# Kernel tuning notes

Measured on AMD Instinct MI355X. Metric: run time of the kernel, lower is better.

Reference implementation:

```python
import jax, jax.numpy as jnp
import numpy as np

N_NODES = 50000
N_EDGES = 800000
IN_FEAT = 1000
HID = 128
HEADS = 2
NEG_SLOPE = 0.2  # PyG GATConv default
EPS = 1e-16      # PyG softmax denom eps


def setup_inputs() -> dict:
    key = jax.random.key(0)
    ks = jax.random.split(key, 12)
    x = jax.random.normal(ks[0], (N_NODES, IN_FEAT), dtype=jnp.float32)
    edge_index = jax.random.randint(ks[1], (2, N_EDGES), 0, N_NODES, dtype=jnp.int64)
    readout_idx = jax.random.randint(ks[2], (1024,), 0, N_NODES, dtype=jnp.int64)
    s = 0.05
    return {
        "x": x,
        "edge_index": edge_index,
        "readout_idx": readout_idx,
        "W1": jax.random.normal(ks[3], (IN_FEAT, HEADS * HID), dtype=jnp.float32) * s,
        "att_src1": jax.random.normal(ks[4], (HEADS, HID), dtype=jnp.float32) * s,
        "att_dst1": jax.random.normal(ks[5], (HEADS, HID), dtype=jnp.float32) * s,
        "b1": jax.random.normal(ks[6], (HEADS * HID,), dtype=jnp.float32) * s,
        "W2": jax.random.normal(ks[7], (HEADS * HID, 1), dtype=jnp.float32) * s,
        "att_src2": jax.random.normal(ks[8], (1, 1), dtype=jnp.float32) * s,
        "att_dst2": jax.random.normal(ks[9], (1, 1), dtype=jnp.float32) * s,
        "b2": jax.random.normal(ks[10], (1,), dtype=jnp.float32) * s,
    }


def gat_conv(x, edge_index, W, att_src, att_dst, bias, heads, out_dim, concat):
    """PyG GATConv with add_self_loops=False. x: [N, F_in]."""
    n = x.shape[0]
    src, dst = edge_index[0], edge_index[1]
    h = (x @ W).reshape(n, heads, out_dim)            # [N, H, D]
    a_src = jnp.einsum("nhd,hd->nh", h, att_src)      # [N, H]
    a_dst = jnp.einsum("nhd,hd->nh", h, att_dst)
    e = jax.nn.leaky_relu(a_src[src] + a_dst[dst], NEG_SLOPE)  # [E, H]
    # softmax over incoming edges of each destination node
    e_max = jax.ops.segment_max(e, dst, num_segments=n)
    e_exp = jnp.exp(e - e_max[dst])
    denom = jax.ops.segment_sum(e_exp, dst, num_segments=n)
    alpha = e_exp / (denom[dst] + EPS)                # [E, H]
    msg = h[src] * alpha[:, :, None]                  # [E, H, D]
    out = jax.ops.segment_sum(msg, dst, num_segments=n)  # [N, H, D]
    out = out.reshape(n, heads * out_dim) if concat else out.mean(axis=1)
    return out + bias


def reference(x, edge_index, readout_idx, W1, att_src1, att_dst1, b1,
              W2, att_src2, att_dst2, b2):
    # dropout is identity in eval mode
    h = gat_conv(x, edge_index, W1, att_src1, att_dst1, b1, HEADS, HID, True)
    h = jax.nn.relu(h)
    out = gat_conv(h, edge_index, W2, att_src2, att_dst2, b2, 1, 1, False)  # [N, 1]
    return out[readout_idx]  # [1024, 1]
```

## Files before the change

kernel.cpp:

```cpp
#include <hip/hip_runtime.h>
#include <hip/hip_bf16.h>
#include <math.h>

#define N_NODES 50000
#define N_EDGES 800000
#define IN_FEAT 1000
#define HID 128
#define HEADS 2
#define FOUT 256
#define NEG_SLOPE 0.2f
#define EPS 1e-16f

#define KPAD 1024
#define GEMM_NWG 782

typedef __bf16 bf16x8 __attribute__((ext_vector_type(8)));
typedef float f32x4 __attribute__((ext_vector_type(4)));

__device__ __forceinline__ float lrelu(float v) { return v > 0.f ? v : NEG_SLOPE * v; }

__device__ __forceinline__ ushort bf16rn(float v) {
  union { float f; unsigned u; } a; a.f = v;
  unsigned r = a.u + 0x7FFFu + ((a.u >> 16) & 1u);
  return (ushort)(r >> 16);
}

__device__ __forceinline__ void gload_lds16(const void* g, void* l) {
  __builtin_amdgcn_global_load_lds((const __attribute__((address_space(1))) void*)g,
                                   (__attribute__((address_space(3))) void*)l, 16, 0, 0);
}

__global__ void hist_kernel(const int* __restrict__ dst, int* __restrict__ counts) {
  int e = blockIdx.x * blockDim.x + threadIdx.x;
  if (e < N_EDGES) atomicAdd(&counts[dst[e]], 1);
}

__global__ __launch_bounds__(1024) void scan1_kernel(const int* __restrict__ counts,
                                                     int* __restrict__ iscan,
                                                     int* __restrict__ bsum) {
  __shared__ int buf[1024];
  const int t = threadIdx.x;
  const int i = blockIdx.x * 1024 + t;
  int v = (i < N_NODES) ? counts[i] : 0;
  buf[t] = v;
  __syncthreads();
#pragma unroll
  for (int off = 1; off < 1024; off <<= 1) {
    int x = (t >= off) ? buf[t - off] : 0;
    __syncthreads();
    buf[t] += x;
    __syncthreads();
  }
  if (i < N_NODES) iscan[i] = buf[t];
  if (t == 1023) bsum[blockIdx.x] = buf[1023];
}

__global__ __launch_bounds__(64) void scan2_kernel(const int* __restrict__ bsum,
                                                   int* __restrict__ boff,
                                                   int* __restrict__ row_start, int nblk) {
  const int t = threadIdx.x;
  int v = (t < nblk) ? bsum[t] : 0;
  int s = v;
#pragma unroll
  for (int off = 1; off < 64; off <<= 1) {
    int y = __shfl_up(s, off, 64);
    if (t >= off) s += y;
  }
  if (t < nblk) boff[t] = s - v;
  if (t == nblk - 1) row_start[N_NODES] = s;
}

__global__ void scan3_kernel(const int* __restrict__ iscan, const int* __restrict__ counts,
                             const int* __restrict__ boff, int* __restrict__ row_start,
                             int* __restrict__ cursor) {
  int i = blockIdx.x * blockDim.x + threadIdx.x;
  if (i < N_NODES) {
    int rs = boff[i >> 10] + iscan[i] - counts[i];
    row_start[i] = rs;
    cursor[i] = rs;
  }
}

__global__ void scatter_kernel(const int* __restrict__ src, const int* __restrict__ dst,
                               int* __restrict__ cursor, int* __restrict__ csr_src) {
  int e = blockIdx.x * blockDim.x + threadIdx.x;
  if (e < N_EDGES) {
    int pos = atomicAdd(&cursor[dst[e]], 1);
    csr_src[pos] = src[e];
  }
}

__global__ __launch_bounds__(256) void cvtB1_kernel(const float* __restrict__ B,
                                                    ushort* __restrict__ Bt) {
  int i = blockIdx.x * 256 + threadIdx.x;
  int nn = i >> 8;
  int k4 = (i & 255) << 2;
  ushort4 h;
#pragma unroll
  for (int j = 0; j < 4; ++j) {
    int k = k4 + j;
    float v = (k < IN_FEAT) ? B[(size_t)k * FOUT + nn] : 0.f;
    ((ushort*)&h)[j] = bf16rn(v);
  }
  *(ushort4*)(Bt + (size_t)nn * KPAD + k4) = h;
}

__global__ __launch_bounds__(256, 2) void gemm_fused2_kernel(
    const float* __restrict__ X, const ushort* __restrict__ Bt,
    float* __restrict__ C) {
  __shared__ ushort lB[2][128 * 64];

  const int orig = blockIdx.x;
  const int q = GEMM_NWG >> 3, r = GEMM_NWG & 7;
  const int xcd = orig & 7, idx = orig >> 3;
  const int lin = (xcd < r) ? xcd * (q + 1) + idx : r * (q + 1) + (xcd - r) * q + idx;
  const int brow = (lin >> 1) * 128;
  const int bcol = (lin & 1) * 128;

  const int t = threadIdx.x;
  const int lane = t & 63, wid = t >> 6;
  const int fr = lane & 15, g = lane >> 4;
  const int wrow = wid * 32;

  float4 areg[2][2][2];

  auto loadA = [&](int ks) {
#pragma unroll
    for (int m = 0; m < 2; ++m)
#pragma unroll
      for (int h = 0; h < 2; ++h) {
        const int row = brow + wrow + m * 16 + fr;
        const int k = ks * 64 + h * 32 + g * 8;
        if (row < N_NODES && k < IN_FEAT) {
          const float* p = X + (size_t)row * IN_FEAT + k;
          areg[m][h][0] = *(const float4*)p;
          areg[m][h][1] = *(const float4*)(p + 4);
        } else {
          areg[m][h][0] = make_float4(0.f, 0.f, 0.f, 0.f);
          areg[m][h][1] = make_float4(0.f, 0.f, 0.f, 0.f);
        }
      }
  };

  auto stageB = [&](int ks, int buf) {
    const int k0b = ks * 128;
#pragma unroll
    for (int i = 0; i < 4; ++i) {
      int u = i * 256 + t;
      int row = u >> 3;
      int inner = (u & 7) * 16;
      int soff = inner ^ ((row & 7) << 4);
      size_t boff = (size_t)(bcol + row) * (KPAD * 2) + k0b + soff;
      gload_lds16((const char*)Bt + boff, (char*)&lB[buf][0] + u * 16);
    }
  };

  f32x4 acc[2][8];
  const f32x4 z4 = {0.f, 0.f, 0.f, 0.f};
#pragma unroll
  for (int m = 0; m < 2; ++m)
#pragma unroll
    for (int n = 0; n < 8; ++n) acc[m][n] = z4;

  stageB(0, 0);
  loadA(0);
  const int NK = KPAD / 64;
  for (int ks = 0; ks < NK; ++ks) {
    bf16x8 ah[2][2], al[2][2];
#pragma unroll
    for (int m = 0; m < 2; ++m)
#pragma unroll
      for (int h = 0; h < 2; ++h) {
        const float* vv = (const float*)&areg[m][h][0];
        bf16x8 hv, lv;
#pragma unroll
        for (int j = 0; j < 8; ++j) {
          float v = vv[j];
          unsigned u = __float_as_uint(v);
          ((ushort*)&hv)[j] = (ushort)(u >> 16);
          float hf = __uint_as_float(u & 0xFFFF0000u);
          float d = v - hf;
          ((ushort*)&lv)[j] = (ushort)(__float_as_uint(d) >> 16);
        }
        ah[m][h] = hv;
        al[m][h] = lv;
      }
    if (ks + 1 < NK) {
      loadA(ks + 1);
      asm volatile("s_waitcnt vmcnt(8)" ::: "memory");
    } else {
      asm volatile("s_waitcnt vmcnt(0)" ::: "memory");
    }
    __builtin_amdgcn_sched_barrier(0);
    __builtin_amdgcn_s_barrier();
    __builtin_amdgcn_sched_barrier(0);
    if (ks + 1 < NK) stageB(ks + 1, (ks + 1) & 1);
    const int buf = ks & 1;
#pragma unroll
    for (int h = 0; h < 2; ++h) {
      bf16x8 bfrag[8];
#pragma unroll
      for (int n = 0; n < 8; ++n) {
        int row = n * 16 + fr;
        int off = row * 128 + ((h * 64 + g * 16) ^ ((row & 7) << 4));
        bfrag[n] = *(const bf16x8*)((const char*)&lB[buf][0] + off);
      }
#pragma unroll
      for (int m = 0; m < 2; ++m)
#pragma unroll
        for (int n = 0; n < 8; ++n) {
          acc[m][n] = __builtin_amdgcn_mfma_f32_16x16x32_bf16(ah[m][h], bfrag[n], acc[m][n], 0, 0, 0);
          acc[m][n] = __builtin_amdgcn_mfma_f32_16x16x32_bf16(al[m][h], bfrag[n], acc[m][n], 0, 0, 0);
        }
    }
  }

#pragma unroll
  for (int m = 0; m < 2; ++m) {
    int rowbase = brow + wrow + m * 16 + g * 4;
#pragma unroll
    for (int n = 0; n < 8; ++n) {
      int col = bcol + n * 16 + fr;
#pragma unroll
      for (int rr = 0; rr < 4; ++rr) {
        int row = rowbase + rr;
        if (row < N_NODES) C[(size_t)row * FOUT + col] = acc[m][n][rr];
      }
    }
  }
}

__global__ __launch_bounds__(64) void att1_kernel(const float* __restrict__ h1,
                                                  const float* __restrict__ as,
                                                  const float* __restrict__ ad,
                                                  float* __restrict__ asrc,
                                                  float* __restrict__ adst) {
  const int n = blockIdx.x;
  const int lane = threadIdx.x;
  const float* hr = h1 + (size_t)n * FOUT;
  float4 hv = *(const float4*)(hr + 4 * lane);
  float4 sv = *(const float4*)(as + 4 * lane);
  float4 dv = *(const float4*)(ad + 4 * lane);
  float ps = hv.x * sv.x + hv.y * sv.y + hv.z * sv.z + hv.w * sv.w;
  float pd = hv.x * dv.x + hv.y * dv.y + hv.z * dv.z + hv.w * dv.w;
#pragma unroll
  for (int off = 16; off > 0; off >>= 1) {
    ps += __shfl_xor(ps, off, 64);
    pd += __shfl_xor(pd, off, 64);
  }
  if ((lane & 31) == 0) {
    int hh = lane >> 5;
    asrc[2 * n + hh] = ps;
    adst[2 * n + hh] = pd;
  }
}

__global__ __launch_bounds__(64) void agg1_kernel(
    const float* __restrict__ h1, const float* __restrict__ asrc,
    const float* __restrict__ adst, const int* __restrict__ row_start,
    const int* __restrict__ csr_src, const float* __restrict__ b1,
    const float* __restrict__ W2, float* __restrict__ z) {
  const int n = blockIdx.x;
  const int lane = threadIdx.x;
  const bool head0 = lane < 32;
  const float ad0 = adst[2 * n], ad1 = adst[2 * n + 1];
  const int jb = row_start[n], je = row_start[n + 1];
  float ax = 0.f, ay = 0.f, az = 0.f, aw = 0.f;
  float m0 = -INFINITY, m1 = -INFINITY, s0 = 0.f, s1 = 0.f;

  for (int base = jb; base < je; base += 64) {
    int cnt = je - base;
    if (cnt > 64) cnt = 64;
    const bool act = lane < cnt;
    const int sr = csr_src[base + (act ? lane : 0)];
    float e0 = -INFINITY, e1 = -INFINITY;
    if (act) {
      const float2 av = *(const float2*)(asrc + 2 * sr);
      e0 = lrelu(av.x + ad0);
      e1 = lrelu(av.y + ad1);
    }
    float c0 = e0, c1 = e1;
#pragma unroll
    for (int off = 32; off > 0; off >>= 1) {
      c0 = fmaxf(c0, __shfl_xor(c0, off, 64));
      c1 = fmaxf(c1, __shfl_xor(c1, off, 64));
    }
    const float m0n = fmaxf(m0, c0), m1n = fmaxf(m1, c1);
    const float f0 = __expf(m0 - m0n), f1 = __expf(m1 - m1n);
    const float p0 = act ? __expf(e0 - m0n) : 0.f;
    const float p1 = act ? __expf(e1 - m1n) : 0.f;
    float t0 = p0, t1 = p1;
#pragma unroll
    for (int off = 32; off > 0; off >>= 1) {
      t0 += __shfl_xor(t0, off, 64);
      t1 += __shfl_xor(t1, off, 64);
    }
    s0 = s0 * f0 + t0;
    s1 = s1 * f1 + t1;
    m0 = m0n;
    m1 = m1n;
    const float f = head0 ? f0 : f1;
    ax *= f; ay *= f; az *= f; aw *= f;
    for (int j = 0; j < cnt; ++j) {
      const int srj = __shfl(sr, j, 64);
      const float pj0 = __shfl(p0, j, 64);
      const float pj1 = __shfl(p1, j, 64);
      const float pj = head0 ? pj0 : pj1;
      float4 hv = *(const float4*)(h1 + (size_t)srj * FOUT + 4 * lane);
      ax = fmaf(pj, hv.x, ax);
      ay = fmaf(pj, hv.y, ay);
      az = fmaf(pj, hv.z, az);
      aw = fmaf(pj, hv.w, aw);
    }
  }
  const float inv = head0 ? 1.f / (s0 + EPS) : 1.f / (s1 + EPS);
  float4 bv = *(const float4*)(b1 + 4 * lane);
  float4 wv = *(const float4*)(W2 + 4 * lane);
  float r0 = fmaxf(fmaf(ax, inv, bv.x), 0.f);
  float r1 = fmaxf(fmaf(ay, inv, bv.y), 0.f);
  float r2 = fmaxf(fmaf(az, inv, bv.z), 0.f);
  float r3 = fmaxf(fmaf(aw, inv, bv.w), 0.f);
  float part = r0 * wv.x + r1 * wv.y + r2 * wv.z + r3 * wv.w;
#pragma unroll
  for (int off = 32; off > 0; off >>= 1) part += __shfl_xor(part, off, 64);
  if (lane == 0) z[n] = part;
}

__global__ __launch_bounds__(64) void agg2_kernel(
    const float* __restrict__ z, const int* __restrict__ row_start,
    const int* __restrict__ csr_src, const float* __restrict__ as2p,
    const float* __restrict__ ad2p, const float* __restrict__ b2p,
    float* __restrict__ out2) {
  const int n = blockIdx.x;
  const int lane = threadIdx.x;
  const float as2 = as2p[0], ad2 = ad2p[0], b2 = b2p[0];
  const float adz = z[n] * ad2;
  const int jb = row_start[n], je = row_start[n + 1];
  float m = -INFINITY, s = 0.f, num = 0.f;
  for (int base = jb; base < je; base += 64) {
    int cnt = je - base;
    if (cnt > 64) cnt = 64;
    const bool act = lane < cnt;
    const int sr = csr_src[base + (act ? lane : 0)];
    const float zs = act ? z[sr] : 0.f;
    const float e = act ? lrelu(zs * as2 + adz) : -INFINITY;
    float c = e;
#pragma unroll
    for (int off = 32; off > 0; off >>= 1) c = fmaxf(c, __shfl_xor(c, off, 64));
    const float mn = fmaxf(m, c);
    const float f = __expf(m - mn);
    const float p = act ? __expf(e - mn) : 0.f;
    float tp = p, tz = p * zs;
#pragma unroll
    for (int off = 32; off > 0; off >>= 1) {
      tp += __shfl_xor(tp, off, 64);
      tz += __shfl_xor(tz, off, 64);
    }
    s = s * f + tp;
    num = num * f + tz;
    m = mn;
  }
  if (lane == 0) out2[n] = num / (s + EPS) + b2;
}

__global__ void readout_kernel(const float* __restrict__ out2, const int* __restrict__ ridx,
                               float* __restrict__ out, int n) {
  int i = blockIdx.x * blockDim.x + threadIdx.x;
  if (i < n) out[i] = out2[ridx[i]];
}

extern "C" void kernel_launch(void* const* d_in, const int* in_sizes, int n_in,
                              void* d_out, int out_size, void* d_ws, size_t ws_size,
                              hipStream_t stream) {
  const float* x   = (const float*)d_in[0];
  const int* ei    = (const int*)d_in[1];
  const int* ridx  = (const int*)d_in[2];
  const float* W1  = (const float*)d_in[3];
  const float* as1 = (const float*)d_in[4];
  const float* ad1 = (const float*)d_in[5];
  const float* b1  = (const float*)d_in[6];
  const float* W2  = (const float*)d_in[7];
  const float* as2 = (const float*)d_in[8];
  const float* ad2 = (const float*)d_in[9];
  const float* b2  = (const float*)d_in[10];
  float* out = (float*)d_out;

  char* ws = (char*)d_ws;
  size_t off = 0;
  auto alloc = [&](size_t bytes) -> void* {
    void* p = ws + off;
    off += (bytes + 255) & ~(size_t)255;
    return p;
  };
  float* h1   = (float*)alloc((size_t)N_NODES * FOUT * 4);
  float* asrc = (float*)alloc((size_t)N_NODES * 2 * 4);
  float* adst = (float*)alloc((size_t)N_NODES * 2 * 4);
  float* z    = (float*)alloc((size_t)N_NODES * 4);
  float* out2 = (float*)alloc((size_t)N_NODES * 4);
  int* counts = (int*)alloc((size_t)N_NODES * 4);
  int* rowst  = (int*)alloc((size_t)(N_NODES + 1) * 4);
  int* cursor = (int*)alloc((size_t)N_NODES * 4);
  int* csr    = (int*)alloc((size_t)N_EDGES * 4);
  int* iscan  = (int*)alloc((size_t)N_NODES * 4);
  int* bsum   = (int*)alloc(64 * 4);
  int* boff   = (int*)alloc(64 * 4);
  ushort* Bt  = (ushort*)alloc((size_t)FOUT * KPAD * 2);

  const int* src = ei;
  const int* dst = ei + N_EDGES;
  const int nblk = (N_NODES + 1023) / 1024;

  hipMemsetAsync(counts, 0, (size_t)N_NODES * 4, stream);
  hist_kernel<<<(N_EDGES + 255) / 256, 256, 0, stream>>>(dst, counts);
  scan1_kernel<<<nblk, 1024, 0, stream>>>(counts, iscan, bsum);
  scan2_kernel<<<1, 64, 0, stream>>>(bsum, boff, rowst, nblk);
  scan3_kernel<<<(N_NODES + 255) / 256, 256, 0, stream>>>(iscan, counts, boff, rowst, cursor);
  scatter_kernel<<<(N_EDGES + 255) / 256, 256, 0, stream>>>(src, dst, cursor, csr);

  cvtB1_kernel<<<256, 256, 0, stream>>>(W1, Bt);
  gemm_fused2_kernel<<<GEMM_NWG, 256, 0, stream>>>(x, Bt, h1);

  att1_kernel<<<N_NODES, 64, 0, stream>>>(h1, as1, ad1, asrc, adst);
  agg1_kernel<<<N_NODES, 64, 0, stream>>>(h1, asrc, adst, rowst, csr, b1, W2, z);
  agg2_kernel<<<N_NODES, 64, 0, stream>>>(z, rowst, csr, as2, ad2, b2, out2);
  readout_kernel<<<4, 256, 0, stream>>>(out2, ridx, out, out_size);
}
```

Baseline: 579.8 us.

## Fuse attention logits into LDS-free GEMM with full-width row tiles

The GEMM drops LDS staging of the bf16 weight tile. Each wave now loads its B fragments straight from global memory with register double-buffering, and the A tile is double-buffered across k steps. Each 512-thread block covers a 128-row by 256-column tile, so every X row is read once instead of twice, which halves the grid. The per-node attention dot products are computed from the accumulators in the epilogue with lane shuffles, so the separate att1 kernel and its re-read of h1 go away. The cost is that B is fetched redundantly from global/L2 by every wave, and the larger block with more live registers may lower occupancy.

```diff
diff --git a/kernel.cpp b/kernel.cpp
--- a/kernel.cpp
+++ b/kernel.cpp
@@ -12,7 +12,7 @@
 #define EPS 1e-16f
 
 #define KPAD 1024
-#define GEMM_NWG 782
+#define GEMM_NWG 391
 
 typedef __bf16 bf16x8 __attribute__((ext_vector_type(8)));
 typedef float f32x4 __attribute__((ext_vector_type(4)));
@@ -23,11 +23,6 @@
   union { float f; unsigned u; } a; a.f = v;
   unsigned r = a.u + 0x7FFFu + ((a.u >> 16) & 1u);
   return (ushort)(r >> 16);
-}
-
-__device__ __forceinline__ void gload_lds16(const void* g, void* l) {
-  __builtin_amdgcn_global_load_lds((const __attribute__((address_space(1))) void*)g,
-                                   (__attribute__((address_space(3))) void*)l, 16, 0, 0);
 }
 
 __global__ void hist_kernel(const int* __restrict__ dst, int* __restrict__ counts) {
@@ -105,56 +100,26 @@
   *(ushort4*)(Bt + (size_t)nn * KPAD + k4) = h;
 }
 
-__global__ __launch_bounds__(256, 2) void gemm_fused2_kernel(
+__global__ __launch_bounds__(512, 2) void gemm_nolds_kernel(
     const float* __restrict__ X, const ushort* __restrict__ Bt,
-    float* __restrict__ C) {
-  __shared__ ushort lB[2][128 * 64];
-
+    const float* __restrict__ as1, const float* __restrict__ ad1,
+    float* __restrict__ C, float* __restrict__ asrc, float* __restrict__ adst) {
+  const int q = GEMM_NWG >> 3, r = GEMM_NWG & 7;
   const int orig = blockIdx.x;
-  const int q = GEMM_NWG >> 3, r = GEMM_NWG & 7;
   const int xcd = orig & 7, idx = orig >> 3;
   const int lin = (xcd < r) ? xcd * (q + 1) + idx : r * (q + 1) + (xcd - r) * q + idx;
-  const int brow = (lin >> 1) * 128;
-  const int bcol = (lin & 1) * 128;
-
-  const int t = threadIdx.x;
-  const int lane = t & 63, wid = t >> 6;
+  const int brow = lin * 128;
+
+  const int t = threadIdx.x, lane = t & 63, wid = t >> 6;
+  const int wc = wid & 1;
+  const int wrow = (wid >> 1) * 32;
   const int fr = lane & 15, g = lane >> 4;
-  const int wrow = wid * 32;
-
-  float4 areg[2][2][2];
-
-  auto loadA = [&](int ks) {
-#pragma unroll
-    for (int m = 0; m < 2; ++m)
-#pragma unroll
-      for (int h = 0; h < 2; ++h) {
-        const int row = brow + wrow + m * 16 + fr;
-        const int k = ks * 64 + h * 32 + g * 8;
-        if (row < N_NODES && k < IN_FEAT) {
-          const float* p = X + (size_t)row * IN_FEAT + k;
-          areg[m][h][0] = *(const float4*)p;
-          areg[m][h][1] = *(const float4*)(p + 4);
-        } else {
-          areg[m][h][0] = make_float4(0.f, 0.f, 0.f, 0.f);
-          areg[m][h][1] = make_float4(0.f, 0.f, 0.f, 0.f);
-        }
-      }
-  };
-
-  auto stageB = [&](int ks, int buf) {
-    const int k0b = ks * 128;
-#pragma unroll
-    for (int i = 0; i < 4; ++i) {
-      int u = i * 256 + t;
-      int row = u >> 3;
-      int inner = (u & 7) * 16;
-      int soff = inner ^ ((row & 7) << 4);
-      size_t boff = (size_t)(bcol + row) * (KPAD * 2) + k0b + soff;
-      gload_lds16((const char*)Bt + boff, (char*)&lB[buf][0] + u * 16);
-    }
-  };
-
+  const int row0 = brow + wrow + fr;
+  const int NK = KPAD / 64;
+
+  float4 aA[2][2][2], aB[2][2][2];
+  bf16x8 bfA[8], bfB[8];
+  bf16x8 ah[2][2], al[2][2];
   f32x4 acc[2][8];
   const f32x4 z4 = {0.f, 0.f, 0.f, 0.f};
 #pragma unroll
@@ -162,16 +127,38 @@
 #pragma unroll
     for (int n = 0; n < 8; ++n) acc[m][n] = z4;
 
-  stageB(0, 0);
-  loadA(0);
-  const int NK = KPAD / 64;
-  for (int ks = 0; ks < NK; ++ks) {
-    bf16x8 ah[2][2], al[2][2];
+  auto loadA = [&](int ks, float4 (&d)[2][2][2]) {
+#pragma unroll
+    for (int m = 0; m < 2; ++m) {
+      int rr = row0 + m * 16;
+      int rc = rr < N_NODES ? rr : N_NODES - 1;
+      const float* base = X + (size_t)rc * IN_FEAT;
+#pragma unroll
+      for (int h = 0; h < 2; ++h) {
+        int k = ks * 64 + h * 32 + g * 8;
+        if (k < IN_FEAT) {
+          d[m][h][0] = *(const float4*)(base + k);
+          d[m][h][1] = *(const float4*)(base + k + 4);
+        } else {
+          d[m][h][0] = make_float4(0.f, 0.f, 0.f, 0.f);
+          d[m][h][1] = make_float4(0.f, 0.f, 0.f, 0.f);
+        }
+      }
+    }
+  };
+  auto loadB = [&](int ks, int h, bf16x8 (&bf)[8]) {
+#pragma unroll
+    for (int n = 0; n < 8; ++n) {
+      const ushort* p = Bt + (size_t)(wc * 128 + n * 16 + fr) * KPAD + ks * 64 + h * 32 + g * 8;
+      bf[n] = *(const bf16x8*)p;
+    }
+  };
+  auto cvt = [&](const float4 (&s)[2][2][2]) {
 #pragma unroll
     for (int m = 0; m < 2; ++m)
 #pragma unroll
       for (int h = 0; h < 2; ++h) {
-        const float* vv = (const float*)&areg[m][h][0];
+        const float* vv = (const float*)&s[m][h][0];
         bf16x8 hv, lv;
 #pragma unroll
         for (int j = 0; j < 8; ++j) {
@@ -179,79 +166,77 @@
           unsigned u = __float_as_uint(v);
           ((ushort*)&hv)[j] = (ushort)(u >> 16);
           float hf = __uint_as_float(u & 0xFFFF0000u);
-          float d = v - hf;
-          ((ushort*)&lv)[j] = (ushort)(__float_as_uint(d) >> 16);
+          ((ushort*)&lv)[j] = (ushort)(__float_as_uint(v - hf) >> 16);
         }
         ah[m][h] = hv;
         al[m][h] = lv;
       }
-    if (ks + 1 < NK) {
-      loadA(ks + 1);
-      asm volatile("s_waitcnt vmcnt(8)" ::: "memory");
-    } else {
-      asm volatile("s_waitcnt vmcnt(0)" ::: "memory");
-    }
-    __builtin_amdgcn_sched_barrier(0);
-    __builtin_amdgcn_s_barrier();
-    __builtin_amdgcn_sched_barrier(0);
-    if (ks + 1 < NK) stageB(ks + 1, (ks + 1) & 1);
-    const int buf = ks & 1;
-#pragma unroll
-    for (int h = 0; h < 2; ++h) {
-      bf16x8 bfrag[8];
+  };
+  auto mmac = [&](int h, bf16x8 (&bf)[8]) {
+#pragma unroll
+    for (int m = 0; m < 2; ++m)
 #pragma unroll
       for (int n = 0; n < 8; ++n) {
-        int row = n * 16 + fr;
-        int off = row * 128 + ((h * 64 + g * 16) ^ ((row & 7) << 4));
-        bfrag[n] = *(const bf16x8*)((const char*)&lB[buf][0] + off);
-      }
-#pragma unroll
-      for (int m = 0; m < 2; ++m)
-#pragma unroll
-        for (int n = 0; n < 8; ++n) {
-          acc[m][n] = __builtin_amdgcn_mfma_f32_16x16x32_bf16(ah[m][h], bfrag[n], acc[m][n], 0, 0, 0);
-          acc[m][n] = __builtin_amdgcn_mfma_f32_16x16x32_bf16(al[m][h], bfrag[n], acc[m][n], 0, 0, 0);
-        }
-    }
-  }
+        acc[m][n] = __builtin_amdgcn_mfma_f32_16x16x32_bf16(ah[m][h], bf[n], acc[m][n], 0, 0, 0);
+        acc[m][n] = __builtin_amdgcn_mfma_f32_16x16x32_bf16(al[m][h], bf[n], acc[m][n], 0, 0, 0);
+      }
+  };
+  auto step = [&](float4 (&cur)[2][2][2], float4 (&nxt)[2][2][2], int ks) {
+    cvt(cur);
+    if (ks + 1 < NK) loadA(ks + 1, nxt);
+    loadB(ks, 1, bfB);
+    mmac(0, bfA);
+    if (ks + 1 < NK) loadB(ks + 1, 0, bfA);
+    mmac(1, bfB);
+  };
+
+  loadA(0, aA);
+  loadB(0, 0, bfA);
+  for (int k2 = 0; k2 < NK; k2 += 2) {
+    step(aA, aB, k2);
+    step(aB, aA, k2 + 1);
+  }
+
+  float ws8[8], wd8[8];
+#pragma unroll
+  for (int n = 0; n < 8; ++n) {
+    ws8[n] = as1[wc * 128 + n * 16 + fr];
+    wd8[n] = ad1[wc * 128 + n * 16 + fr];
+  }
+#pragma unroll
+  for (int m = 0; m < 2; ++m)
+#pragma unroll
+    for (int rr = 0; rr < 4; ++rr) {
+      float ls = 0.f, ld = 0.f;
+#pragma unroll
+      for (int n = 0; n < 8; ++n) {
+        ls = fmaf(acc[m][n][rr], ws8[n], ls);
+        ld = fmaf(acc[m][n][rr], wd8[n], ld);
+      }
+#pragma unroll
+      for (int off = 1; off < 16; off <<= 1) {
+        ls += __shfl_xor(ls, off, 64);
+        ld += __shfl_xor(ld, off, 64);
+      }
+      int row = brow + wrow + m * 16 + g * 4 + rr;
+      if (fr == 0 && row < N_NODES) {
+        asrc[2 * row + wc] = ls;
+        adst[2 * row + wc] = ld;
+      }
+    }
 
 #pragma unroll
   for (int m = 0; m < 2; ++m) {
-    int rowbase = brow + wrow + m * 16 + g * 4;
+    int rowb = brow + wrow + m * 16 + g * 4;
 #pragma unroll
     for (int n = 0; n < 8; ++n) {
-      int col = bcol + n * 16 + fr;
+      int col = wc * 128 + n * 16 + fr;
 #pragma unroll
       for (int rr = 0; rr < 4; ++rr) {
-        int row = rowbase + rr;
+        int row = rowb + rr;
         if (row < N_NODES) C[(size_t)row * FOUT + col] = acc[m][n][rr];
       }
     }
-  }
-}
-
-__global__ __launch_bounds__(64) void att1_kernel(const float* __restrict__ h1,
-                                                  const float* __restrict__ as,
-                                                  const float* __restrict__ ad,
-                                                  float* __restrict__ asrc,
-                                                  float* __restrict__ adst) {
-  const int n = blockIdx.x;
-  const int lane = threadIdx.x;
-  const float* hr = h1 + (size_t)n * FOUT;
-  float4 hv = *(const float4*)(hr + 4 * lane);
-  float4 sv = *(const float4*)(as + 4 * lane);
-  float4 dv = *(const float4*)(ad + 4 * lane);
-  float ps = hv.x * sv.x + hv.y * sv.y + hv.z * sv.z + hv.w * sv.w;
-  float pd = hv.x * dv.x + hv.y * dv.y + hv.z * dv.z + hv.w * dv.w;
-#pragma unroll
-  for (int off = 16; off > 0; off >>= 1) {
-    ps += __shfl_xor(ps, off, 64);
-    pd += __shfl_xor(pd, off, 64);
-  }
-  if ((lane & 31) == 0) {
-    int hh = lane >> 5;
-    asrc[2 * n + hh] = ps;
-    adst[2 * n + hh] = pd;
   }
 }
 
@@ -418,9 +403,8 @@
   scatter_kernel<<<(N_EDGES + 255) / 256, 256, 0, stream>>>(src, dst, cursor, csr);
 
   cvtB1_kernel<<<256, 256, 0, stream>>>(W1, Bt);
-  gemm_fused2_kernel<<<GEMM_NWG, 256, 0, stream>>>(x, Bt, h1);
-
-  att1_kernel<<<N_NODES, 64, 0, stream>>>(h1, as1, ad1, asrc, adst);
+  gemm_nolds_kernel<<<GEMM_NWG, 512, 0, stream>>>(x, Bt, as1, ad1, h1, asrc, adst);
+
   agg1_kernel<<<N_NODES, 64, 0, stream>>>(h1, asrc, adst, rowst, csr, b1, W2, z);
   agg2_kernel<<<N_NODES, 64, 0, stream>>>(z, rowst, csr, as2, ad2, b2, out2);
   readout_kernel<<<4, 256, 0, stream>>>(out2, ridx, out, out_size);
```

Result: slower. 640.7 us (+10.5%).
